# Optimization experiments

Hardware: AMD Instinct MI355X
Metric: run time of the kernel (lower is better)

The kernel has to match this reference:

```python
import jax, jax.numpy as jnp
import numpy as np

N = 10000
E = 640000
C = 128   # in_channels
H = 512   # hidden_dim
O = 128   # out_channels


def setup_inputs() -> dict:
    key = jax.random.key(0)
    k1, k2, k3, k4, k5, k6, k7 = jax.random.split(key, 7)
    x = jax.random.normal(k1, (N, C), dtype=jnp.float32)
    edge_index = jax.random.randint(k2, (2, E), 0, N, dtype=jnp.int64)
    # MLP params (Linear(2C, H) -> ReLU -> Linear(H, O)), torch default init scale
    w1 = jax.random.uniform(k3, (2 * C, H), jnp.float32, -1, 1) / np.sqrt(2 * C)
    b1 = jax.random.uniform(k4, (H,), jnp.float32, -1, 1) / np.sqrt(2 * C)
    w2 = jax.random.uniform(k5, (H, O), jnp.float32, -1, 1) / np.sqrt(H)
    b2 = jax.random.uniform(k6, (O,), jnp.float32, -1, 1) / np.sqrt(H)
    return {"x": x, "edge_index": edge_index, "w1": w1, "b1": b1, "w2": w2, "b2": b2}


def reference(x, edge_index, w1, b1, w2, b2):
    row, col = edge_index[0], edge_index[1]
    # scatter_mean: mean of source features x[col] into destination row
    summed = jax.ops.segment_sum(x[col], row, num_segments=N)          # [N, C]
    count = jax.ops.segment_sum(jnp.ones((E,), x.dtype), row, num_segments=N)
    neighbor_mean = summed / jnp.maximum(count, 1.0)[:, None]          # [N, C]
    h = jnp.concatenate([x, neighbor_mean], axis=1)                    # [N, 2C]
    h = jax.nn.relu(h @ w1 + b1)                                       # [N, H]
    return h @ w2 + b2                                                 # [N, O]
```

## Files before the change

kernel.cpp:

```cpp
#include <hip/hip_runtime.h>

#define C_IN 128
#define H_DIM 512
#define O_DIM 128
#define CAP   192
#define PAD   16

typedef __attribute__((ext_vector_type(8))) short short8;
typedef __attribute__((ext_vector_type(4))) float f32x4;

__device__ inline unsigned short f2bf(float f) {
    unsigned int u = __float_as_uint(f);
    unsigned int r = (u + 0x7FFF + ((u >> 16) & 1)) >> 16;
    return (unsigned short)r;
}
__device__ inline float bf2f(unsigned short s) {
    return __uint_as_float(((unsigned int)s) << 16);
}

__device__ inline void tr_tile(const float* __restrict__ src, unsigned short* __restrict__ dst,
                               int R, int Ccols, int bx, int by) {
    __shared__ float tile[32][33];
    const int c0 = bx * 32, r0 = by * 32;
    const int tx = threadIdx.x & 31, ty = threadIdx.x >> 5;
#pragma unroll
    for (int i = 0; i < 32; i += 8)
        tile[ty + i][tx] = src[(long)(r0 + ty + i) * Ccols + c0 + tx];
    __syncthreads();
#pragma unroll
    for (int i = 0; i < 32; i += 8)
        dst[(long)(c0 + ty + i) * R + r0 + tx] = f2bf(tile[tx][ty + i]);
}

__global__ __launch_bounds__(256)
void prep_kernel(const float* __restrict__ w1, unsigned short* __restrict__ w1t,
                 const float* __restrict__ w2, unsigned short* __restrict__ w2t,
                 const float* __restrict__ x, unsigned short* __restrict__ h0,
                 int* __restrict__ cnt_p, int N) {
    if (blockIdx.z == 0) {
        if (blockIdx.y < (2 * C_IN) / 32) tr_tile(w1, w1t, 2 * C_IN, H_DIM, blockIdx.x, blockIdx.y);
    } else if (blockIdx.z == 1) {
        if (blockIdx.x < O_DIM / 32) tr_tile(w2, w2t, H_DIM, O_DIM, blockIdx.x, blockIdx.y);
    } else {
        const int bid = blockIdx.y * 16 + blockIdx.x;
        const int gtid = bid * 256 + threadIdx.x;
        const int nf4 = N * C_IN / 4;
        for (int i = gtid; i < nf4; i += 65536) {
            int n = i >> 5, c4 = i & 31;
            float4 v = ((const float4*)x)[i];
            ushort4 s;
            s.x = f2bf(v.x); s.y = f2bf(v.y); s.z = f2bf(v.z); s.w = f2bf(v.w);
            *(ushort4*)(h0 + (long)n * (2 * C_IN) + c4 * 4) = s;
        }
        const int n4 = N * PAD / 4;
        for (int i = gtid; i < n4; i += 65536)
            ((int4*)cnt_p)[i] = make_int4(0, 0, 0, 0);
    }
}

__global__ void fill_kernel(const int* __restrict__ ei, int* __restrict__ cnt_p,
                            unsigned short* __restrict__ bucket, int E) {
    int e = blockIdx.x * blockDim.x + threadIdx.x;
    if (e >= E) return;
    int row = ei[e];
    int col = ei[E + e];
    int slot = atomicAdd(&cnt_p[row * PAD], 1);
    if (slot < CAP) bucket[(long)row * CAP + slot] = (unsigned short)col;
}

__global__ __launch_bounds__(256)
void gather_kernel(const unsigned short* __restrict__ bucket,
                   const int* __restrict__ cnt_p, unsigned short* __restrict__ h0,
                   int N) {
    const int lane = threadIdx.x & 63;
    const int n = blockIdx.x * 4 + (threadIdx.x >> 6);
    if (n >= N) return;
    const int half = lane >> 5;
    const int l32 = lane & 31;
    const int degt = cnt_p[n * PAD];
    const int deg = min(degt, CAP);
    const long base = (long)n * CAP;

    float a0 = 0.f, a1 = 0.f, a2 = 0.f, a3 = 0.f;
    int e = 0;
    for (; e + 4 <= deg; e += 4) {
        int c0 = bucket[base + e + half];
        int c1 = bucket[base + e + 2 + half];
        ushort4 u0 = *(const ushort4*)(h0 + (long)c0 * (2 * C_IN) + l32 * 4);
        ushort4 u1 = *(const ushort4*)(h0 + (long)c1 * (2 * C_IN) + l32 * 4);
        a0 += bf2f(u0.x) + bf2f(u1.x);
        a1 += bf2f(u0.y) + bf2f(u1.y);
        a2 += bf2f(u0.z) + bf2f(u1.z);
        a3 += bf2f(u0.w) + bf2f(u1.w);
    }
    for (; e + 2 <= deg; e += 2) {
        int c = bucket[base + e + half];
        ushort4 u = *(const ushort4*)(h0 + (long)c * (2 * C_IN) + l32 * 4);
        a0 += bf2f(u.x); a1 += bf2f(u.y); a2 += bf2f(u.z); a3 += bf2f(u.w);
    }
    if (e < deg && half == 0) {
        int c = bucket[base + e];
        ushort4 u = *(const ushort4*)(h0 + (long)c * (2 * C_IN) + l32 * 4);
        a0 += bf2f(u.x); a1 += bf2f(u.y); a2 += bf2f(u.z); a3 += bf2f(u.w);
    }
    a0 += __shfl_xor(a0, 32, 64);
    a1 += __shfl_xor(a1, 32, 64);
    a2 += __shfl_xor(a2, 32, 64);
    a3 += __shfl_xor(a3, 32, 64);

    if (half == 0) {
        float inv = 1.0f / fmaxf((float)degt, 1.0f);
        ushort4 mv;
        mv.x = f2bf(a0 * inv);
        mv.y = f2bf(a1 * inv);
        mv.z = f2bf(a2 * inv);
        mv.w = f2bf(a3 * inv);
        *(ushort4*)(h0 + (long)n * (2 * C_IN) + C_IN + l32 * 4) = mv;
    }
}

template <bool RELU, bool OUT_BF16>
__global__ __launch_bounds__(256)
void gemm_mfma(const unsigned short* __restrict__ A, const unsigned short* __restrict__ Bt,
               const float* __restrict__ bias, void* __restrict__ Cmat,
               int M, int K, int Nw) {
    __shared__ __align__(16) unsigned short As[64][72];
    __shared__ __align__(16) unsigned short Bs[64][72];

    const int t = threadIdx.x;
    const int m0 = blockIdx.y * 64;
    const int n0 = blockIdx.x * 64;

    const int lane = t & 63;
    const int w = t >> 6;
    const int wm = (w >> 1) * 32;
    const int wn = (w & 1) * 32;
    const int l16 = lane & 15;
    const int q8 = (lane >> 4) * 8;

    const int sr = t >> 3;
    const int sc = (t & 7) * 8;

    f32x4 acc[2][2] = {};

    for (int k0 = 0; k0 < K; k0 += 64) {
        {
            int gm = m0 + sr;
            short8 v = {};
            if (gm < M) v = *(const short8*)(A + (long)gm * K + k0 + sc);
            *(short8*)&As[sr][sc] = v;
            gm = m0 + sr + 32;
            short8 v2 = {};
            if (gm < M) v2 = *(const short8*)(A + (long)gm * K + k0 + sc);
            *(short8*)&As[sr + 32][sc] = v2;
        }
        {
            int gn = n0 + sr;
            *(short8*)&Bs[sr][sc] = *(const short8*)(Bt + (long)gn * K + k0 + sc);
            gn = n0 + sr + 32;
            *(short8*)&Bs[sr + 32][sc] = *(const short8*)(Bt + (long)gn * K + k0 + sc);
        }
        __syncthreads();

#pragma unroll
        for (int kk = 0; kk < 64; kk += 32) {
            short8 a0 = *(const short8*)&As[wm + l16][kk + q8];
            short8 a1 = *(const short8*)&As[wm + 16 + l16][kk + q8];
            short8 b0 = *(const short8*)&Bs[wn + l16][kk + q8];
            short8 b1 = *(const short8*)&Bs[wn + 16 + l16][kk + q8];
            acc[0][0] = __builtin_amdgcn_mfma_f32_16x16x32_bf16(a0, b0, acc[0][0], 0, 0, 0);
            acc[0][1] = __builtin_amdgcn_mfma_f32_16x16x32_bf16(a0, b1, acc[0][1], 0, 0, 0);
            acc[1][0] = __builtin_amdgcn_mfma_f32_16x16x32_bf16(a1, b0, acc[1][0], 0, 0, 0);
            acc[1][1] = __builtin_amdgcn_mfma_f32_16x16x32_bf16(a1, b1, acc[1][1], 0, 0, 0);
        }
        __syncthreads();
    }

    const int rbase = (lane >> 4) * 4;
#pragma unroll
    for (int mi = 0; mi < 2; mi++) {
#pragma unroll
        for (int ni = 0; ni < 2; ni++) {
            int gn = n0 + wn + ni * 16 + l16;
            float bb = bias[gn];
#pragma unroll
            for (int r = 0; r < 4; r++) {
                int gm = m0 + wm + mi * 16 + rbase + r;
                if (gm >= M) continue;
                float v = acc[mi][ni][r] + bb;
                if (RELU) v = fmaxf(v, 0.f);
                if (OUT_BF16)
                    ((unsigned short*)Cmat)[(long)gm * Nw + gn] = f2bf(v);
                else
                    ((float*)Cmat)[(long)gm * Nw + gn] = v;
            }
        }
    }
}

extern "C" void kernel_launch(void* const* d_in, const int* in_sizes, int n_in,
                              void* d_out, int out_size, void* d_ws, size_t ws_size,
                              hipStream_t stream) {
    const float* x  = (const float*)d_in[0];
    const int*   ei = (const int*)d_in[1];
    const float* w1 = (const float*)d_in[2];
    const float* b1 = (const float*)d_in[3];
    const float* w2 = (const float*)d_in[4];
    const float* b2 = (const float*)d_in[5];
    float* out = (float*)d_out;

    const int N = in_sizes[0] / C_IN;
    const int E = in_sizes[1] / 2;

    unsigned short* h0b = (unsigned short*)d_ws;
    unsigned short* h1b = h0b + (size_t)N * (2 * C_IN);
    unsigned short* w1t = h1b + (size_t)N * H_DIM;
    unsigned short* w2t = w1t + (size_t)H_DIM * (2 * C_IN);
    int* cnt_p = (int*)(w2t + (size_t)O_DIM * H_DIM);
    unsigned short* bucket = (unsigned short*)(cnt_p + (size_t)N * PAD);

    prep_kernel<<<dim3(16, 16, 3), 256, 0, stream>>>(w1, w1t, w2, w2t, x, h0b, cnt_p, N);
    fill_kernel<<<(E + 255) / 256, 256, 0, stream>>>(ei, cnt_p, bucket, E);
    gather_kernel<<<(N + 3) / 4, 256, 0, stream>>>(bucket, cnt_p, h0b, N);

    dim3 g1(H_DIM / 64, (N + 63) / 64);
    gemm_mfma<true, true><<<g1, 256, 0, stream>>>(h0b, w1t, b1, h1b, N, 2 * C_IN, H_DIM);

    dim3 g2(O_DIM / 64, (N + 63) / 64);
    gemm_mfma<false, false><<<g2, 256, 0, stream>>>(h1b, w2t, b2, out, N, H_DIM, O_DIM);
}
```

Before: 145.6 us.

## Fuse both MLP GEMMs into one kernel keeping hidden activations in LDS

Replaces the two separate tiled MFMA GEMM launches with a single fused kernel that processes 32-row tiles. Each block holds its A rows in registers, streams W1 in 32-column chunks through shared memory, writes ReLU'd bf16 hidden activations to LDS, and then runs the second GEMM reading W2 directly from global memory. This removes the round trip of the N x 512 hidden buffer through global memory and one kernel launch. In exchange it uses fewer, larger blocks (313), more syncs per block, and uncached global W2 loads, which may limit occupancy and MFMA throughput.

Result: no change. 146.8 us (+0.9%).

```diff
diff --git a/kernel.cpp b/kernel.cpp
--- a/kernel.cpp
+++ b/kernel.cpp
@@ -5,6 +5,7 @@
 #define O_DIM 128
 #define CAP   192
 #define PAD   16
+#define BM    32
 
 typedef __attribute__((ext_vector_type(8))) short short8;
 typedef __attribute__((ext_vector_type(4))) float f32x4;
@@ -119,80 +120,93 @@
     }
 }
 
-template <bool RELU, bool OUT_BF16>
 __global__ __launch_bounds__(256)
-void gemm_mfma(const unsigned short* __restrict__ A, const unsigned short* __restrict__ Bt,
-               const float* __restrict__ bias, void* __restrict__ Cmat,
-               int M, int K, int Nw) {
-    __shared__ __align__(16) unsigned short As[64][72];
-    __shared__ __align__(16) unsigned short Bs[64][72];
+void fused_mlp(const unsigned short* __restrict__ h0,
+               const unsigned short* __restrict__ w1t,
+               const float* __restrict__ b1,
+               const unsigned short* __restrict__ w2t,
+               const float* __restrict__ b2,
+               float* __restrict__ out, int M) {
+    __shared__ __align__(16) unsigned short Bs[32][264];
+    __shared__ __align__(16) unsigned short h1s[32][520];
 
     const int t = threadIdx.x;
-    const int m0 = blockIdx.y * 64;
-    const int n0 = blockIdx.x * 64;
-
+    const int m0 = blockIdx.x * BM;
     const int lane = t & 63;
     const int w = t >> 6;
-    const int wm = (w >> 1) * 32;
-    const int wn = (w & 1) * 32;
     const int l16 = lane & 15;
-    const int q8 = (lane >> 4) * 8;
-
-    const int sr = t >> 3;
-    const int sc = (t & 7) * 8;
-
-    f32x4 acc[2][2] = {};
-
-    for (int k0 = 0; k0 < K; k0 += 64) {
+    const int q = lane >> 4;
+    const int q8 = q * 8;
+
+    const int mf1 = w >> 1;
+    const int nf1 = w & 1;
+
+    short8 a_reg[8];
+    {
+        int gm = m0 + mf1 * 16 + l16;
+        if (gm < M) {
+            const unsigned short* ap = h0 + (long)gm * (2 * C_IN) + q8;
+#pragma unroll
+            for (int s = 0; s < 8; s++) a_reg[s] = *(const short8*)(ap + s * 32);
+        } else {
+#pragma unroll
+            for (int s = 0; s < 8; s++) a_reg[s] = short8{};
+        }
+    }
+
+    for (int nc = 0; nc < 16; nc++) {
         {
-            int gm = m0 + sr;
-            short8 v = {};
-            if (gm < M) v = *(const short8*)(A + (long)gm * K + k0 + sc);
-            *(short8*)&As[sr][sc] = v;
-            gm = m0 + sr + 32;
-            short8 v2 = {};
-            if (gm < M) v2 = *(const short8*)(A + (long)gm * K + k0 + sc);
-            *(short8*)&As[sr + 32][sc] = v2;
+            const unsigned short* src = w1t + (long)nc * 32 * 256;
+#pragma unroll
+            for (int i = 0; i < 4; i++) {
+                int cid = t + i * 256;
+                int r = cid >> 5, c8 = (cid & 31) * 8;
+                *(short8*)&Bs[r][c8] = *(const short8*)(src + r * 256 + c8);
+            }
+        }
+        __syncthreads();
+        f32x4 acc = {};
+#pragma unroll
+        for (int s = 0; s < 8; s++) {
+            short8 b = *(const short8*)&Bs[nf1 * 16 + l16][s * 32 + q8];
+            acc = __builtin_amdgcn_mfma_f32_16x16x32_bf16(a_reg[s], b, acc, 0, 0, 0);
         }
         {
-            int gn = n0 + sr;
-            *(short8*)&Bs[sr][sc] = *(const short8*)(Bt + (long)gn * K + k0 + sc);
-            gn = n0 + sr + 32;
-            *(short8*)&Bs[sr + 32][sc] = *(const short8*)(Bt + (long)gn * K + k0 + sc);
+            int coll = nf1 * 16 + l16;
+            float bb = b1[nc * 32 + coll];
+#pragma unroll
+            for (int r = 0; r < 4; r++) {
+                int m = mf1 * 16 + q * 4 + r;
+                float v = fmaxf(acc[r] + bb, 0.f);
+                h1s[m][nc * 32 + coll] = f2bf(v);
+            }
         }
         __syncthreads();
-
-#pragma unroll
-        for (int kk = 0; kk < 64; kk += 32) {
-            short8 a0 = *(const short8*)&As[wm + l16][kk + q8];
-            short8 a1 = *(const short8*)&As[wm + 16 + l16][kk + q8];
-            short8 b0 = *(const short8*)&Bs[wn + l16][kk + q8];
-            short8 b1 = *(const short8*)&Bs[wn + 16 + l16][kk + q8];
-            acc[0][0] = __builtin_amdgcn_mfma_f32_16x16x32_bf16(a0, b0, acc[0][0], 0, 0, 0);
-            acc[0][1] = __builtin_amdgcn_mfma_f32_16x16x32_bf16(a0, b1, acc[0][1], 0, 0, 0);
-            acc[1][0] = __builtin_amdgcn_mfma_f32_16x16x32_bf16(a1, b0, acc[1][0], 0, 0, 0);
-            acc[1][1] = __builtin_amdgcn_mfma_f32_16x16x32_bf16(a1, b1, acc[1][1], 0, 0, 0);
-        }
-        __syncthreads();
-    }
-
-    const int rbase = (lane >> 4) * 4;
-#pragma unroll
-    for (int mi = 0; mi < 2; mi++) {
-#pragma unroll
-        for (int ni = 0; ni < 2; ni++) {
-            int gn = n0 + wn + ni * 16 + l16;
-            float bb = bias[gn];
+    }
+
+    f32x4 acc2[2][2] = {};
+    const int wn = w * 32;
+#pragma unroll
+    for (int ks = 0; ks < 16; ks++) {
+        short8 a0 = *(const short8*)&h1s[l16][ks * 32 + q8];
+        short8 a1 = *(const short8*)&h1s[16 + l16][ks * 32 + q8];
+        short8 b0 = *(const short8*)(w2t + (long)(wn + l16) * H_DIM + ks * 32 + q8);
+        short8 b1v = *(const short8*)(w2t + (long)(wn + 16 + l16) * H_DIM + ks * 32 + q8);
+        acc2[0][0] = __builtin_amdgcn_mfma_f32_16x16x32_bf16(a0, b0, acc2[0][0], 0, 0, 0);
+        acc2[0][1] = __builtin_amdgcn_mfma_f32_16x16x32_bf16(a0, b1v, acc2[0][1], 0, 0, 0);
+        acc2[1][0] = __builtin_amdgcn_mfma_f32_16x16x32_bf16(a1, b0, acc2[1][0], 0, 0, 0);
+        acc2[1][1] = __builtin_amdgcn_mfma_f32_16x16x32_bf16(a1, b1v, acc2[1][1], 0, 0, 0);
+    }
+#pragma unroll
+    for (int mf = 0; mf < 2; mf++) {
+#pragma unroll
+        for (int nf = 0; nf < 2; nf++) {
+            int gn = wn + nf * 16 + l16;
+            float bb = b2[gn];
 #pragma unroll
             for (int r = 0; r < 4; r++) {
-                int gm = m0 + wm + mi * 16 + rbase + r;
-                if (gm >= M) continue;
-                float v = acc[mi][ni][r] + bb;
-                if (RELU) v = fmaxf(v, 0.f);
-                if (OUT_BF16)
-                    ((unsigned short*)Cmat)[(long)gm * Nw + gn] = f2bf(v);
-                else
-                    ((float*)Cmat)[(long)gm * Nw + gn] = v;
+                int gm = m0 + mf * 16 + q * 4 + r;
+                if (gm < M) out[(long)gm * O_DIM + gn] = acc2[mf][nf][r] + bb;
             }
         }
     }
@@ -213,8 +227,7 @@
     const int E = in_sizes[1] / 2;
 
     unsigned short* h0b = (unsigned short*)d_ws;
-    unsigned short* h1b = h0b + (size_t)N * (2 * C_IN);
-    unsigned short* w1t = h1b + (size_t)N * H_DIM;
+    unsigned short* w1t = h0b + (size_t)N * (2 * C_IN);
     unsigned short* w2t = w1t + (size_t)H_DIM * (2 * C_IN);
     int* cnt_p = (int*)(w2t + (size_t)O_DIM * H_DIM);
     unsigned short* bucket = (unsigned short*)(cnt_p + (size_t)N * PAD);
@@ -222,10 +235,5 @@
     prep_kernel<<<dim3(16, 16, 3), 256, 0, stream>>>(w1, w1t, w2, w2t, x, h0b, cnt_p, N);
     fill_kernel<<<(E + 255) / 256, 256, 0, stream>>>(ei, cnt_p, bucket, E);
     gather_kernel<<<(N + 3) / 4, 256, 0, stream>>>(bucket, cnt_p, h0b, N);
-
-    dim3 g1(H_DIM / 64, (N + 63) / 64);
-    gemm_mfma<true, true><<<g1, 256, 0, stream>>>(h0b, w1t, b1, h1b, N, 2 * C_IN, H_DIM);
-
-    dim3 g2(O_DIM / 64, (N + 63) / 64);
-    gemm_mfma<false, false><<<g2, 256, 0, stream>>>(h1b, w2t, b2, out, N, H_DIM, O_DIM);
-}
+    fused_mlp<<<(N + BM - 1) / BM, 256, 0, stream>>>(h0b, w1t, b1, w2t, b2, out, N);
+}
```
